# Kernel optimization log

Measured on AMD Instinct MI355X. Metric: run time of the kernel, lower is better.

The kernel has to match this reference:

```python
import jax, jax.numpy as jnp
import numpy as np

N_NODES = 100000
N_EDGES = 1600000
DK = 32
OUT_DIM = 32


def setup_inputs() -> dict:
    key = jax.random.key(0)
    ks = jax.random.split(key, 7)
    X = jax.random.normal(ks[0], (N_NODES, DK), dtype=jnp.float32)
    K = jax.random.normal(ks[1], (N_NODES, DK), dtype=jnp.float32)
    V = jax.random.normal(ks[2], (N_NODES, DK), dtype=jnp.float32)
    # output projection (nn.Dense(out_dim)) params
    W_o = jax.random.normal(ks[3], (DK, OUT_DIM), dtype=jnp.float32) / np.sqrt(DK)
    b_o = jnp.zeros((OUT_DIM,), dtype=jnp.float32)
    # sparsity descriptor td: edge list, dst sorted so segment ops see sorted ids
    src = jax.random.randint(ks[4], (N_EDGES,), 0, N_NODES, dtype=jnp.int32)
    dst = jnp.sort(jax.random.randint(ks[5], (N_EDGES,), 0, N_NODES, dtype=jnp.int32))
    return {"X": X, "K": K, "V": V, "W_o": W_o, "b_o": b_o,
            "src": src, "dst": dst, "num_seg": N_NODES}


def reference(X, K, V, W_o, b_o, src, dst, num_seg):
    dk = X.shape[-1]
    # per-edge attention logits: <Q[dst], K[src]> / dk  -> (E,)
    scores = jnp.einsum('ed,ed->e', jnp.take(X, dst, axis=0),
                        jnp.take(K, src, axis=0)) / dk
    # segment (per-neighborhood) softmax over edges sharing a dst node
    seg_max = jax.ops.segment_max(scores, dst, num_segments=num_seg,
                                  indices_are_sorted=True)
    e = jnp.exp(scores - jnp.take(seg_max, dst))
    denom = jax.ops.segment_sum(e, dst, num_segments=num_seg,
                                indices_are_sorted=True)
    alpha = e / jnp.take(denom, dst)  # (E,)
    # weighted aggregation of values, scattered back to nodes -> (N, dk)
    agg = jax.ops.segment_sum(alpha[:, None] * jnp.take(V, src, axis=0), dst,
                              num_segments=num_seg, indices_are_sorted=True)
    # output projection W_o
    return agg @ W_o + b_o
```

## Files before the change

kernel.cpp:

```cpp
#include <hip/hip_runtime.h>
#include <math.h>

#define DK 32
#define OUT_DIM 32

__global__ void build_row_ptr_kernel(const int* __restrict__ dst, int E, int N,
                                     int* __restrict__ row_ptr) {
    int e = blockIdx.x * blockDim.x + threadIdx.x;
    if (e >= E) return;
    int cur  = dst[e];
    int prev = (e == 0) ? -1 : dst[e - 1];
    for (int j = prev + 1; j <= cur; ++j) row_ptr[j] = e;
    if (e == E - 1) {
        for (int j = cur + 1; j <= N; ++j) row_ptr[j] = E;
    }
}

__global__ __launch_bounds__(256) void gat_node_kernel(
    const float* __restrict__ X, const float* __restrict__ Km,
    const float* __restrict__ Vm, const float* __restrict__ Wo,
    const float* __restrict__ bo, const int* __restrict__ src,
    const int* __restrict__ row_ptr, float* __restrict__ out, int N) {

    const int tid  = threadIdx.x;
    const int wave = tid >> 6;
    const int lane = tid & 63;
    const int g    = lane >> 3;
    const int c    = lane & 7;
    const int j    = lane & 31;
    const int half = lane >> 5;

    const int n = blockIdx.x * 4 + wave;
    if (n >= N) return;

    const int begin = row_ptr[n];
    const int end   = row_ptr[n + 1];

    const float4* X4 = (const float4*)X;
    const float4* K4 = (const float4*)Km;
    const float4* V4 = (const float4*)Vm;

    const float4 q4 = X4[n * 8 + c];

    float  l   = 0.0f;
    float4 acc = make_float4(0.0f, 0.0f, 0.0f, 0.0f);

    for (int e0 = begin; e0 < end; e0 += 16) {
        const int  ea = e0 + g;
        const int  eb = ea + 8;
        const bool va = ea < end;
        const bool vb = eb < end;
        const int sa = src[min(ea, end - 1)];
        const int sb = src[min(eb, end - 1)];
        const float4 ka  = K4[sa * 8 + c];
        const float4 kb  = K4[sb * 8 + c];
        const float4 vva = V4[sa * 8 + c];
        const float4 vvb = V4[sb * 8 + c];

        float pa = fmaf(ka.x, q4.x, fmaf(ka.y, q4.y, fmaf(ka.z, q4.z, ka.w * q4.w)));
        float pb = fmaf(kb.x, q4.x, fmaf(kb.y, q4.y, fmaf(kb.z, q4.z, kb.w * q4.w)));
        pa += __shfl_xor(pa, 1);  pb += __shfl_xor(pb, 1);
        pa += __shfl_xor(pa, 2);  pb += __shfl_xor(pb, 2);
        pa += __shfl_xor(pa, 4);  pb += __shfl_xor(pb, 4);

        const float wa = va ? __expf(pa * 0.03125f) : 0.0f;
        const float wb = vb ? __expf(pb * 0.03125f) : 0.0f;

        l += wa + wb;
        acc.x = fmaf(wa, vva.x, acc.x);  acc.y = fmaf(wa, vva.y, acc.y);
        acc.z = fmaf(wa, vva.z, acc.z);  acc.w = fmaf(wa, vva.w, acc.w);
        acc.x = fmaf(wb, vvb.x, acc.x);  acc.y = fmaf(wb, vvb.y, acc.y);
        acc.z = fmaf(wb, vvb.z, acc.z);  acc.w = fmaf(wb, vvb.w, acc.w);
    }

#pragma unroll
    for (int m = 8; m <= 32; m <<= 1) {
        l     += __shfl_xor(l, m);
        acc.x += __shfl_xor(acc.x, m);
        acc.y += __shfl_xor(acc.y, m);
        acc.z += __shfl_xor(acc.z, m);
        acc.w += __shfl_xor(acc.w, m);
    }

    const float inv = (end > begin) ? (1.0f / l) : 0.0f;

    float ag[4] = {acc.x, acc.y, acc.z, acc.w};
    float s = 0.0f;
#pragma unroll
    for (int k = 0; k < 32; ++k) {
        const float a = __int_as_float(
            __builtin_amdgcn_readlane(__float_as_int(ag[k & 3]), k >> 2));
        s = fmaf(a, Wo[k * OUT_DIM + j], s);
    }
    if (half == 0) {
        out[n * OUT_DIM + j] = fmaf(s, inv, bo[j]);
    }
}

extern "C" void kernel_launch(void* const* d_in, const int* in_sizes, int n_in,
                              void* d_out, int out_size, void* d_ws, size_t ws_size,
                              hipStream_t stream) {
    const float* X  = (const float*)d_in[0];
    const float* Km = (const float*)d_in[1];
    const float* Vm = (const float*)d_in[2];
    const float* Wo = (const float*)d_in[3];
    const float* bo = (const float*)d_in[4];
    const int* src  = (const int*)d_in[5];
    const int* dst  = (const int*)d_in[6];

    const int N = in_sizes[0] / DK;
    const int E = in_sizes[5];

    int* row_ptr = (int*)d_ws;
    float* out   = (float*)d_out;

    const int tb = 256;
    build_row_ptr_kernel<<<(E + tb - 1) / tb, tb, 0, stream>>>(dst, E, N, row_ptr);

    const int nodes_per_block = 4;
    const int grid = (N + nodes_per_block - 1) / nodes_per_block;
    gat_node_kernel<<<grid, 256, 0, stream>>>(X, Km, Vm, Wo, bo, src, row_ptr, out, N);
}
```

Before: 155.2 us.

## Repack K and V into interleaved bf16 pairs and process several nodes per wave

Adds a pre-pass that rounds K and V to bf16 and interleaves them into one 32-bit word per element, so each edge needs one 16-byte gather instead of two 16-byte gathers. This halves the random-access gather traffic. The main kernel now handles four nodes per wave and keeps the W_o column in registers, with the 1/dk scale folded into q. The trade-offs are an extra repack kernel per call and reduced precision for K and V. The old fp32 path remains as a fallback when the workspace is too small.

Measured after the change: 157.8 us. No clear change (+1.7%).

```diff
diff --git a/kernel.cpp b/kernel.cpp
--- a/kernel.cpp
+++ b/kernel.cpp
@@ -3,6 +3,7 @@
 
 #define DK 32
 #define OUT_DIM 32
+#define NODES_PER_WAVE 4
 
 __global__ void build_row_ptr_kernel(const int* __restrict__ dst, int E, int N,
                                      int* __restrict__ row_ptr) {
@@ -16,11 +17,24 @@
     }
 }
 
-__global__ __launch_bounds__(256) void gat_node_kernel(
-    const float* __restrict__ X, const float* __restrict__ Km,
-    const float* __restrict__ Vm, const float* __restrict__ Wo,
-    const float* __restrict__ bo, const int* __restrict__ src,
-    const int* __restrict__ row_ptr, float* __restrict__ out, int N) {
+__device__ __forceinline__ unsigned f2bf_rne(float x) {
+    unsigned u = __float_as_uint(x);
+    return (u + 0x7fffu + ((u >> 16) & 1u)) >> 16;
+}
+
+__global__ void repack_kv_kernel(const float* __restrict__ K,
+                                 const float* __restrict__ V,
+                                 unsigned* __restrict__ KV, int total) {
+    int i = blockIdx.x * blockDim.x + threadIdx.x;
+    if (i >= total) return;
+    KV[i] = (f2bf_rne(V[i]) << 16) | f2bf_rne(K[i]);
+}
+
+__global__ __launch_bounds__(256) void gat_node_kv_kernel(
+    const float* __restrict__ X, const uint4* __restrict__ KV,
+    const float* __restrict__ Wo, const float* __restrict__ bo,
+    const int* __restrict__ src, const int* __restrict__ row_ptr,
+    float* __restrict__ out, int N) {
 
     const int tid  = threadIdx.x;
     const int wave = tid >> 6;
@@ -30,21 +44,113 @@
     const int j    = lane & 31;
     const int half = lane >> 5;
 
+    const int n0 = (blockIdx.x * 4 + wave) * NODES_PER_WAVE;
+    if (n0 >= N) return;
+
+    float wcol[32];
+#pragma unroll
+    for (int k = 0; k < 32; ++k) wcol[k] = Wo[k * OUT_DIM + j];
+    const float bj = bo[j];
+
+    const float4* X4 = (const float4*)X;
+
+    for (int i = 0; i < NODES_PER_WAVE; ++i) {
+        const int n = n0 + i;
+        if (n >= N) break;
+        const int begin = row_ptr[n];
+        const int end   = row_ptr[n + 1];
+
+        float4 q4 = X4[n * 8 + c];
+        q4.x *= 0.03125f; q4.y *= 0.03125f;
+        q4.z *= 0.03125f; q4.w *= 0.03125f;
+
+        float  l   = 0.0f;
+        float4 acc = make_float4(0.0f, 0.0f, 0.0f, 0.0f);
+
+        for (int e0 = begin; e0 < end; e0 += 16) {
+            const int  ea = e0 + g;
+            const int  eb = ea + 8;
+            const int  sa = src[min(ea, end - 1)];
+            const int  sb = src[min(eb, end - 1)];
+            const uint4 A = KV[sa * 8 + c];
+            const uint4 B = KV[sb * 8 + c];
+
+            const float ka0 = __uint_as_float(A.x << 16);
+            const float ka1 = __uint_as_float(A.y << 16);
+            const float ka2 = __uint_as_float(A.z << 16);
+            const float ka3 = __uint_as_float(A.w << 16);
+            const float kb0 = __uint_as_float(B.x << 16);
+            const float kb1 = __uint_as_float(B.y << 16);
+            const float kb2 = __uint_as_float(B.z << 16);
+            const float kb3 = __uint_as_float(B.w << 16);
+
+            float pa = fmaf(ka0, q4.x, fmaf(ka1, q4.y, fmaf(ka2, q4.z, ka3 * q4.w)));
+            float pb = fmaf(kb0, q4.x, fmaf(kb1, q4.y, fmaf(kb2, q4.z, kb3 * q4.w)));
+            pa += __shfl_xor(pa, 1);  pb += __shfl_xor(pb, 1);
+            pa += __shfl_xor(pa, 2);  pb += __shfl_xor(pb, 2);
+            pa += __shfl_xor(pa, 4);  pb += __shfl_xor(pb, 4);
+
+            const float wa = (ea < end) ? __expf(pa) : 0.0f;
+            const float wb = (eb < end) ? __expf(pb) : 0.0f;
+            l += wa + wb;
+
+            acc.x = fmaf(wa, __uint_as_float(A.x & 0xffff0000u), acc.x);
+            acc.y = fmaf(wa, __uint_as_float(A.y & 0xffff0000u), acc.y);
+            acc.z = fmaf(wa, __uint_as_float(A.z & 0xffff0000u), acc.z);
+            acc.w = fmaf(wa, __uint_as_float(A.w & 0xffff0000u), acc.w);
+            acc.x = fmaf(wb, __uint_as_float(B.x & 0xffff0000u), acc.x);
+            acc.y = fmaf(wb, __uint_as_float(B.y & 0xffff0000u), acc.y);
+            acc.z = fmaf(wb, __uint_as_float(B.z & 0xffff0000u), acc.z);
+            acc.w = fmaf(wb, __uint_as_float(B.w & 0xffff0000u), acc.w);
+        }
+
+#pragma unroll
+        for (int m = 8; m <= 32; m <<= 1) {
+            l     += __shfl_xor(l, m);
+            acc.x += __shfl_xor(acc.x, m);
+            acc.y += __shfl_xor(acc.y, m);
+            acc.z += __shfl_xor(acc.z, m);
+            acc.w += __shfl_xor(acc.w, m);
+        }
+
+        const float inv = (end > begin) ? (1.0f / l) : 0.0f;
+
+        float ag[4] = {acc.x, acc.y, acc.z, acc.w};
+        float s = 0.0f;
+#pragma unroll
+        for (int k = 0; k < 32; ++k) {
+            const float a = __int_as_float(
+                __builtin_amdgcn_readlane(__float_as_int(ag[k & 3]), k >> 2));
+            s = fmaf(a, wcol[k], s);
+        }
+        if (half == 0) {
+            out[n * OUT_DIM + j] = fmaf(s, inv, bj);
+        }
+    }
+}
+
+__global__ __launch_bounds__(256) void gat_node_f32_kernel(
+    const float* __restrict__ X, const float* __restrict__ Km,
+    const float* __restrict__ Vm, const float* __restrict__ Wo,
+    const float* __restrict__ bo, const int* __restrict__ src,
+    const int* __restrict__ row_ptr, float* __restrict__ out, int N) {
+    const int tid  = threadIdx.x;
+    const int wave = tid >> 6;
+    const int lane = tid & 63;
+    const int g    = lane >> 3;
+    const int c    = lane & 7;
+    const int j    = lane & 31;
+    const int half = lane >> 5;
     const int n = blockIdx.x * 4 + wave;
     if (n >= N) return;
-
     const int begin = row_ptr[n];
     const int end   = row_ptr[n + 1];
-
     const float4* X4 = (const float4*)X;
     const float4* K4 = (const float4*)Km;
     const float4* V4 = (const float4*)Vm;
-
     const float4 q4 = X4[n * 8 + c];
-
     float  l   = 0.0f;
     float4 acc = make_float4(0.0f, 0.0f, 0.0f, 0.0f);
-
     for (int e0 = begin; e0 < end; e0 += 16) {
         const int  ea = e0 + g;
         const int  eb = ea + 8;
@@ -56,23 +162,19 @@
         const float4 kb  = K4[sb * 8 + c];
         const float4 vva = V4[sa * 8 + c];
         const float4 vvb = V4[sb * 8 + c];
-
         float pa = fmaf(ka.x, q4.x, fmaf(ka.y, q4.y, fmaf(ka.z, q4.z, ka.w * q4.w)));
         float pb = fmaf(kb.x, q4.x, fmaf(kb.y, q4.y, fmaf(kb.z, q4.z, kb.w * q4.w)));
         pa += __shfl_xor(pa, 1);  pb += __shfl_xor(pb, 1);
         pa += __shfl_xor(pa, 2);  pb += __shfl_xor(pb, 2);
         pa += __shfl_xor(pa, 4);  pb += __shfl_xor(pb, 4);
-
         const float wa = va ? __expf(pa * 0.03125f) : 0.0f;
         const float wb = vb ? __expf(pb * 0.03125f) : 0.0f;
-
         l += wa + wb;
         acc.x = fmaf(wa, vva.x, acc.x);  acc.y = fmaf(wa, vva.y, acc.y);
         acc.z = fmaf(wa, vva.z, acc.z);  acc.w = fmaf(wa, vva.w, acc.w);
         acc.x = fmaf(wb, vvb.x, acc.x);  acc.y = fmaf(wb, vvb.y, acc.y);
         acc.z = fmaf(wb, vvb.z, acc.z);  acc.w = fmaf(wb, vvb.w, acc.w);
     }
-
 #pragma unroll
     for (int m = 8; m <= 32; m <<= 1) {
         l     += __shfl_xor(l, m);
@@ -81,9 +183,7 @@
         acc.z += __shfl_xor(acc.z, m);
         acc.w += __shfl_xor(acc.w, m);
     }
-
     const float inv = (end > begin) ? (1.0f / l) : 0.0f;
-
     float ag[4] = {acc.x, acc.y, acc.z, acc.w};
     float s = 0.0f;
 #pragma unroll
@@ -112,12 +212,24 @@
     const int E = in_sizes[5];
 
     int* row_ptr = (int*)d_ws;
-    float* out   = (float*)d_out;
+    const size_t kv_off = (((size_t)(N + 1) * 4) + 127) & ~(size_t)127;
+    unsigned* KV = (unsigned*)((char*)d_ws + kv_off);
+    const size_t need = kv_off + (size_t)N * DK * 4;
+    float* out = (float*)d_out;
 
     const int tb = 256;
     build_row_ptr_kernel<<<(E + tb - 1) / tb, tb, 0, stream>>>(dst, E, N, row_ptr);
 
-    const int nodes_per_block = 4;
-    const int grid = (N + nodes_per_block - 1) / nodes_per_block;
-    gat_node_kernel<<<grid, 256, 0, stream>>>(X, Km, Vm, Wo, bo, src, row_ptr, out, N);
-}
+    if (ws_size >= need) {
+        const int total = N * DK;
+        repack_kv_kernel<<<(total + tb - 1) / tb, tb, 0, stream>>>(Km, Vm, KV, total);
+        const int waves = (N + NODES_PER_WAVE - 1) / NODES_PER_WAVE;
+        const int grid  = (waves + 3) / 4;
+        gat_node_kv_kernel<<<grid, 256, 0, stream>>>(X, (const uint4*)KV, Wo, bo,
+                                                     src, row_ptr, out, N);
+    } else {
+        const int grid = (N + 3) / 4;
+        gat_node_f32_kernel<<<grid, 256, 0, stream>>>(X, Km, Vm, Wo, bo,
+                                                      src, row_ptr, out, N);
+    }
+}
```
